# Kernel optimization log

Measured on AMD Instinct MI355X. Metric: run time of the kernel, lower is better.

## Reference

```python
import jax, jax.numpy as jnp
import numpy as np

I, H, O, T = 512, 2048, 512, 4096

def setup_inputs() -> dict:
    key = jax.random.key(0)
    ks = jax.random.split(key, 7)
    s = 0.02  # small init scale to avoid gate saturation
    return {
        "input_seq": jax.random.normal(ks[0], (T, I), dtype=jnp.float32),
        "W_ih": jax.random.normal(ks[1], (4 * H, I), dtype=jnp.float32) * s,
        "W_hh": jax.random.normal(ks[2], (4 * H, H), dtype=jnp.float32) * s,
        "b_ih": jax.random.normal(ks[3], (4 * H,), dtype=jnp.float32) * s,
        "b_hh": jax.random.normal(ks[4], (4 * H,), dtype=jnp.float32) * s,
        "W_lin": jax.random.normal(ks[5], (O, H), dtype=jnp.float32) * s,
        "b_lin": jax.random.normal(ks[6], (O,), dtype=jnp.float32) * s,
    }

def reference(input_seq, W_ih, W_hh, b_ih, b_hh, W_lin, b_lin):
    # Single-layer LSTM, batch=1, initial (h, c) = 0; PyTorch gate order i,f,g,o.
    b = b_ih + b_hh
    # Precompute input projections for all timesteps: (T, 4H)
    xz = input_seq @ W_ih.T + b

    def step(carry, xz_t):
        h, c = carry
        z = xz_t + h @ W_hh.T  # (4H,)
        i, f, g, o = jnp.split(z, 4)
        i = jax.nn.sigmoid(i)
        f = jax.nn.sigmoid(f)
        g = jnp.tanh(g)
        o = jax.nn.sigmoid(o)
        c = f * c + i * g
        h = o * jnp.tanh(c)
        return (h, c), None

    h0 = jnp.zeros((H,), dtype=input_seq.dtype)
    c0 = jnp.zeros((H,), dtype=input_seq.dtype)
    (hT, _), _ = jax.lax.scan(step, (h0, c0), xz)
    # predictions[-1] == linear(lstm_out[-1]) == linear(h_T)
    return hT @ W_lin.T + b_lin
```

## Files before the change

kernel.cpp:

```cpp
#include <hip/hip_runtime.h>


#define TSTEPS 4096
#define HDIM   2048
#define GDIM   8192
#define IDIM   512
#define ODIM   512

#define XZ_BYTES ((size_t)TSTEPS * GDIM * sizeof(float))
#define FLAG_STRIDE 16

__device__ __forceinline__ float sigmoidf_fast(float x) {
    return 1.0f / (1.0f + __expf(-x));
}
__device__ __forceinline__ float tanhf_fast(float x) {
    return 2.0f / (1.0f + __expf(-2.0f * x)) - 1.0f;
}

__global__ __launch_bounds__(256) void xz_gemm(
    const float* __restrict__ A, const float* __restrict__ B,
    const float* __restrict__ bih, const float* __restrict__ bhh,
    float* __restrict__ C)
{
    __shared__ float As[16][132];
    __shared__ float Bs[16][132];

    const int tid = threadIdx.x;
    const int m0 = blockIdx.y * 128;
    const int n0 = blockIdx.x * 128;
    const int tx = tid & 15;
    const int ty = tid >> 4;

    const int lrow  = tid >> 1;
    const int kbase = (tid & 1) * 8;

    float acc[8][8] = {};

    for (int k0 = 0; k0 < IDIM; k0 += 16) {
        const float4 av0 = *(const float4*)(A + (size_t)(m0 + lrow) * IDIM + k0 + kbase);
        const float4 av1 = *(const float4*)(A + (size_t)(m0 + lrow) * IDIM + k0 + kbase + 4);
        const float4 bv0 = *(const float4*)(B + (size_t)(n0 + lrow) * IDIM + k0 + kbase);
        const float4 bv1 = *(const float4*)(B + (size_t)(n0 + lrow) * IDIM + k0 + kbase + 4);

        __syncthreads();
        As[kbase + 0][lrow] = av0.x; As[kbase + 1][lrow] = av0.y;
        As[kbase + 2][lrow] = av0.z; As[kbase + 3][lrow] = av0.w;
        As[kbase + 4][lrow] = av1.x; As[kbase + 5][lrow] = av1.y;
        As[kbase + 6][lrow] = av1.z; As[kbase + 7][lrow] = av1.w;
        Bs[kbase + 0][lrow] = bv0.x; Bs[kbase + 1][lrow] = bv0.y;
        Bs[kbase + 2][lrow] = bv0.z; Bs[kbase + 3][lrow] = bv0.w;
        Bs[kbase + 4][lrow] = bv1.x; Bs[kbase + 5][lrow] = bv1.y;
        Bs[kbase + 6][lrow] = bv1.z; Bs[kbase + 7][lrow] = bv1.w;
        __syncthreads();

#pragma unroll
        for (int kk = 0; kk < 16; ++kk) {
            const float4 a0 = *(const float4*)&As[kk][ty * 8];
            const float4 a1 = *(const float4*)&As[kk][ty * 8 + 4];
            const float4 b0 = *(const float4*)&Bs[kk][tx * 8];
            const float4 b1 = *(const float4*)&Bs[kk][tx * 8 + 4];
            const float ar[8] = {a0.x, a0.y, a0.z, a0.w, a1.x, a1.y, a1.z, a1.w};
            const float br[8] = {b0.x, b0.y, b0.z, b0.w, b1.x, b1.y, b1.z, b1.w};
#pragma unroll
            for (int i = 0; i < 8; ++i)
#pragma unroll
                for (int jj = 0; jj < 8; ++jj)
                    acc[i][jj] = fmaf(ar[i], br[jj], acc[i][jj]);
        }
    }

    float bias[8];
#pragma unroll
    for (int jj = 0; jj < 8; ++jj) {
        const int n = n0 + tx * 8 + jj;
        bias[jj] = bih[n] + bhh[n];
    }
#pragma unroll
    for (int i = 0; i < 8; ++i) {
        float* crow = C + (size_t)(m0 + ty * 8 + i) * GDIM + n0 + tx * 8;
        float4 v0, v1;
        v0.x = acc[i][0] + bias[0]; v0.y = acc[i][1] + bias[1];
        v0.z = acc[i][2] + bias[2]; v0.w = acc[i][3] + bias[3];
        v1.x = acc[i][4] + bias[4]; v1.y = acc[i][5] + bias[5];
        v1.z = acc[i][6] + bias[6]; v1.w = acc[i][7] + bias[7];
        ((float4*)crow)[0] = v0;
        ((float4*)crow)[1] = v1;
    }
}

__global__ __launch_bounds__(256, 1) void lstm_rec(
    const float* __restrict__ Whh, const float* __restrict__ xz,
    float* __restrict__ hbuf, unsigned* __restrict__ flags)
{
    __shared__ float hsh[8 * 260];

    const int tidb = threadIdx.x;
    const int tid  = blockIdx.x * 256 + tidb;
    const int j    = tid >> 5;
    const int g    = (tid >> 3) & 3;
    const int ck   = tid & 7;
    const int row  = g * HDIM + j;
    const int wv   = tidb >> 6;
    const int ln   = tidb & 63;

    const float4* wsrc = (const float4*)(Whh + (size_t)row * HDIM + ck * 256);
    float4 w[64];
#pragma unroll
    for (int i = 0; i < 64; ++i) w[i] = wsrc[i];

    const bool owner = (tid & 31) == 0;
    float cstate = 0.0f;

    const unsigned* myflag = flags + (size_t)(wv * 64 + ln) * FLAG_STRIDE;

    float zx = xz[row];

    for (int t = 0; t < TSTEPS; ++t) {
        {
            const unsigned need = (unsigned)t;
            unsigned spins = 0;
            while (__hip_atomic_load(myflag, __ATOMIC_RELAXED,
                                     __HIP_MEMORY_SCOPE_AGENT) < need) {
                __builtin_amdgcn_s_sleep(1);
                if (++spins > (1u << 22)) break;
            }
        }

        const float* hsrc = hbuf + ((t & 1) << 11) + wv * 512;
        float hv[8];
#pragma unroll
        for (int m = 0; m < 8; ++m)
            hv[m] = __hip_atomic_load(hsrc + m * 64 + ln, __ATOMIC_RELAXED,
                                      __HIP_MEMORY_SCOPE_AGENT);
#pragma unroll
        for (int m = 0; m < 8; ++m) {
            const int k = wv * 512 + m * 64 + ln;
            hsh[(k >> 8) * 260 + (k & 255)] = hv[m];
        }
        __syncthreads();

        const float4* hr = (const float4*)(hsh + ck * 260);
        float a0 = 0.f, a1 = 0.f, a2 = 0.f, a3 = 0.f;
#pragma unroll
        for (int i = 0; i < 64; ++i) {
            const float4 h4 = hr[i];
            a0 = fmaf(w[i].x, h4.x, a0);
            a1 = fmaf(w[i].y, h4.y, a1);
            a2 = fmaf(w[i].z, h4.z, a2);
            a3 = fmaf(w[i].w, h4.w, a3);
        }
        float d = (a0 + a1) + (a2 + a3);
        d += __shfl_xor(d, 1);
        d += __shfl_xor(d, 2);
        d += __shfl_xor(d, 4);
        const float z  = d + zx;
        const float zf = __shfl_xor(z, 8);
        const float zg = __shfl_xor(z, 16);
        const float zo = __shfl_xor(z, 24);

        if (owner) {
            const float ig = sigmoidf_fast(z);
            const float fg = sigmoidf_fast(zf);
            const float gg = tanhf_fast(zg);
            const float og = sigmoidf_fast(zo);
            cstate = fmaf(fg, cstate, ig * gg);
            const float hval = og * tanhf_fast(cstate);
            __hip_atomic_store(hbuf + (((t + 1) & 1) << 11) + j, hval,
                               __ATOMIC_RELAXED, __HIP_MEMORY_SCOPE_AGENT);
        }

        const int tn = (t + 1 < TSTEPS) ? (t + 1) : (TSTEPS - 1);
        zx = xz[(size_t)tn * GDIM + row];

        __syncthreads();
        if (tidb == 0)
            __hip_atomic_store(flags + (size_t)blockIdx.x * FLAG_STRIDE,
                               (unsigned)(t + 1), __ATOMIC_RELAXED,
                               __HIP_MEMORY_SCOPE_AGENT);
    }
}

__global__ __launch_bounds__(256) void final_linear(
    const float* __restrict__ Wlin, const float* __restrict__ blin,
    const float* __restrict__ hT, float* __restrict__ out)
{
    const int wid  = (blockIdx.x * 256 + threadIdx.x) >> 6;
    const int lane = threadIdx.x & 63;
    const float4* wr = (const float4*)(Wlin + (size_t)wid * HDIM);
    const float4* hp = (const float4*)hT;
    float acc = 0.f;
#pragma unroll
    for (int i = 0; i < 8; ++i) {
        const float4 w4 = wr[lane + 64 * i];
        const float4 h4 = hp[lane + 64 * i];
        acc += w4.x * h4.x + w4.y * h4.y + w4.z * h4.z + w4.w * h4.w;
    }
#pragma unroll
    for (int off = 32; off > 0; off >>= 1) acc += __shfl_down(acc, off);
    if (lane == 0) out[wid] = acc + blin[wid];
}

extern "C" void kernel_launch(void* const* d_in, const int* in_sizes, int n_in,
                              void* d_out, int out_size, void* d_ws, size_t ws_size,
                              hipStream_t stream) {
    const float* input = (const float*)d_in[0];
    const float* Wih   = (const float*)d_in[1];
    const float* Whh   = (const float*)d_in[2];
    const float* bih   = (const float*)d_in[3];
    const float* bhh   = (const float*)d_in[4];
    const float* Wlin  = (const float*)d_in[5];
    const float* blin  = (const float*)d_in[6];
    float* out = (float*)d_out;

    char* ws = (char*)d_ws;
    float*    xz    = (float*)ws;
    float*    hbuf  = (float*)(ws + XZ_BYTES);
    unsigned* flags = (unsigned*)(ws + XZ_BYTES + 2 * HDIM * sizeof(float));

    hipMemsetAsync(hbuf, 0,
                   2 * HDIM * sizeof(float) + 256 * FLAG_STRIDE * sizeof(unsigned),
                   stream);

    dim3 ggrid(GDIM / 128, TSTEPS / 128);
    xz_gemm<<<ggrid, 256, 0, stream>>>(input, Wih, bih, bhh, xz);

    lstm_rec<<<dim3(256), dim3(256), 0, stream>>>(Whh, xz, hbuf, flags);

    final_linear<<<ODIM / 4, 256, 0, stream>>>(Wlin, blin, hbuf, out);
}
```

Measured before the change: 18.03 ms.

## Remap LSTM recurrence threads so each wave reads only its own h slice

Changes the thread-to-work mapping in the recurrent kernel. Each wave now owns a 512-wide k-chunk of h that it loaded itself, so the first block barrier before the dot product is removed. Partial sums go through a double-buffered shared array, and a single barrier per step precedes wave 0 computing the gates. Wave 0 also issues the flag store right after a waitcnt instead of after a second barrier, which shortens the per-step critical path. The cost is that gate math and the xz prefetch are serialized on one wave, and the ordering of the h stores before the flag now relies on the waitcnt.

```diff
diff --git a/kernel.cpp b/kernel.cpp
--- a/kernel.cpp
+++ b/kernel.cpp
@@ -92,30 +92,36 @@
     const float* __restrict__ Whh, const float* __restrict__ xz,
     float* __restrict__ hbuf, unsigned* __restrict__ flags)
 {
-    __shared__ float hsh[8 * 260];
+    __shared__ float hsh[4 * 520];
+    __shared__ float part[2][4][32];
 
     const int tidb = threadIdx.x;
-    const int tid  = blockIdx.x * 256 + tidb;
-    const int j    = tid >> 5;
-    const int g    = (tid >> 3) & 3;
-    const int ck   = tid & 7;
-    const int row  = g * HDIM + j;
+    const int b    = blockIdx.x;
     const int wv   = tidb >> 6;
     const int ln   = tidb & 63;
-
-    const float4* wsrc = (const float4*)(Whh + (size_t)row * HDIM + ck * 256);
+    const int sub  = ln >> 5;
+    const int ck   = 2 * wv + sub;
+    const int go   = ln & 31;
+    const int gq   = go >> 3;
+    const int jo   = go & 7;
+    const int j0   = 8 * b;
+    const int row  = gq * HDIM + j0 + jo;
+
+    const float4* wsrc = (const float4*)(Whh + (size_t)row * HDIM) + ck * 64;
     float4 w[64];
 #pragma unroll
     for (int i = 0; i < 64; ++i) w[i] = wsrc[i];
 
-    const bool owner = (tid & 31) == 0;
     float cstate = 0.0f;
 
     const unsigned* myflag = flags + (size_t)(wv * 64 + ln) * FLAG_STRIDE;
 
-    float zx = xz[row];
+    float zx = 0.0f;
+    if (wv == 0) zx = xz[row];
 
     for (int t = 0; t < TSTEPS; ++t) {
+        const int p = t & 1;
+
         {
             const unsigned need = (unsigned)t;
             unsigned spins = 0;
@@ -126,20 +132,18 @@
             }
         }
 
-        const float* hsrc = hbuf + ((t & 1) << 11) + wv * 512;
+        const float* hsrc = hbuf + (p << 11) + wv * 512;
         float hv[8];
 #pragma unroll
         for (int m = 0; m < 8; ++m)
             hv[m] = __hip_atomic_load(hsrc + m * 64 + ln, __ATOMIC_RELAXED,
                                       __HIP_MEMORY_SCOPE_AGENT);
-#pragma unroll
-        for (int m = 0; m < 8; ++m) {
-            const int k = wv * 512 + m * 64 + ln;
-            hsh[(k >> 8) * 260 + (k & 255)] = hv[m];
-        }
-        __syncthreads();
-
-        const float4* hr = (const float4*)(hsh + ck * 260);
+
+#pragma unroll
+        for (int m = 0; m < 8; ++m)
+            hsh[wv * 520 + m * 64 + ln] = hv[m];
+
+        const float4* hr = (const float4*)(hsh + wv * 520 + sub * 256);
         float a0 = 0.f, a1 = 0.f, a2 = 0.f, a3 = 0.f;
 #pragma unroll
         for (int i = 0; i < 64; ++i) {
@@ -150,33 +154,36 @@
             a3 = fmaf(w[i].w, h4.w, a3);
         }
         float d = (a0 + a1) + (a2 + a3);
-        d += __shfl_xor(d, 1);
-        d += __shfl_xor(d, 2);
-        d += __shfl_xor(d, 4);
-        const float z  = d + zx;
-        const float zf = __shfl_xor(z, 8);
-        const float zg = __shfl_xor(z, 16);
-        const float zo = __shfl_xor(z, 24);
-
-        if (owner) {
-            const float ig = sigmoidf_fast(z);
-            const float fg = sigmoidf_fast(zf);
-            const float gg = tanhf_fast(zg);
-            const float og = sigmoidf_fast(zo);
-            cstate = fmaf(fg, cstate, ig * gg);
-            const float hval = og * tanhf_fast(cstate);
-            __hip_atomic_store(hbuf + (((t + 1) & 1) << 11) + j, hval,
-                               __ATOMIC_RELAXED, __HIP_MEMORY_SCOPE_AGENT);
-        }
-
-        const int tn = (t + 1 < TSTEPS) ? (t + 1) : (TSTEPS - 1);
-        zx = xz[(size_t)tn * GDIM + row];
+        d += __shfl_xor(d, 32);
+        if (ln < 32) part[p][wv][ln] = d;
 
         __syncthreads();
-        if (tidb == 0)
-            __hip_atomic_store(flags + (size_t)blockIdx.x * FLAG_STRIDE,
-                               (unsigned)(t + 1), __ATOMIC_RELAXED,
-                               __HIP_MEMORY_SCOPE_AGENT);
+
+        if (wv == 0) {
+            const float z = part[p][0][go] + part[p][1][go] +
+                            part[p][2][go] + part[p][3][go] + zx;
+            const float zf = __shfl(z,  8 + jo);
+            const float zg = __shfl(z, 16 + jo);
+            const float zo = __shfl(z, 24 + jo);
+            if (ln < 8) {
+                const float ig = sigmoidf_fast(z);
+                const float fg = sigmoidf_fast(zf);
+                const float gg = tanhf_fast(zg);
+                const float og = sigmoidf_fast(zo);
+                cstate = fmaf(fg, cstate, ig * gg);
+                const float hval = og * tanhf_fast(cstate);
+                __hip_atomic_store(hbuf + (((t + 1) & 1) << 11) + j0 + jo,
+                                   hval, __ATOMIC_RELAXED,
+                                   __HIP_MEMORY_SCOPE_AGENT);
+            }
+            __builtin_amdgcn_s_waitcnt(0);
+            if (ln == 0)
+                __hip_atomic_store(flags + (size_t)b * FLAG_STRIDE,
+                                   (unsigned)(t + 1), __ATOMIC_RELAXED,
+                                   __HIP_MEMORY_SCOPE_AGENT);
+            const int tn = (t + 1 < TSTEPS) ? (t + 1) : (TSTEPS - 1);
+            zx = xz[(size_t)tn * GDIM + row];
+        }
     }
 }
 
```

Result: slower. 18.91 ms (+4.9%).
